# Performance work log

Hardware: AMD Instinct MI355X
Metric: run time of the kernel (lower is better)

## Reference

```python
import jax, jax.numpy as jnp
import numpy as np

B, OP, MA, F_IN, F_OUT = 8, 400, 200, 64, 64


def setup_inputs() -> dict:
    key = jax.random.key(0)
    ks = jax.random.split(key, 8)
    x = jax.random.normal(ks[0], (B, OP, F_IN), dtype=jnp.float32)
    y = jax.random.normal(ks[1], (B, MA, F_IN), dtype=jnp.float32)
    z = jax.random.normal(ks[2], (B, OP, MA, F_IN), dtype=jnp.float32)
    op_ma_adj = jax.random.randint(ks[3], (B, OP, MA), 0, 2, dtype=jnp.int32)
    # xavier-uniform-ish params
    lim = float(np.sqrt(6.0 / (F_IN + F_OUT)))
    W_op = jax.random.uniform(ks[4], (F_IN, F_OUT), minval=-lim, maxval=lim, dtype=jnp.float32)
    W_ma = jax.random.uniform(ks[5], (F_IN, F_OUT), minval=-lim, maxval=lim, dtype=jnp.float32)
    W_edge = jax.random.uniform(ks[6], (F_IN, F_OUT), minval=-lim, maxval=lim, dtype=jnp.float32)
    lim_a = float(np.sqrt(6.0 / (1 + 3 * F_OUT)))
    att_vec = jax.random.uniform(ks[7], (3 * F_OUT,), minval=-lim_a, maxval=lim_a, dtype=jnp.float32)
    return {"x": x, "y": y, "z": z, "op_ma_adj": op_ma_adj,
            "W_op": W_op, "W_ma": W_ma, "W_edge": W_edge, "att_vec": att_vec}


def reference(x, y, z, op_ma_adj, W_op, W_ma, W_edge, att_vec):
    F = W_op.shape[1]
    h_op = jnp.einsum('bni,io->bno', x, W_op)                      # [B, op, F]
    h = jnp.einsum('bmi,io->bmo', y, W_ma)                         # [B, ma, F]
    h_edge = jnp.einsum('bnmi,io->bnmo', z, W_edge).transpose(0, 2, 1, 3)  # [B, ma, op, F]
    # attention score: concat([h_op, h_ma, h_edge]) @ a  ==  per-part dot products (no BxMAxOPx3F materialization)
    a_op, a_ma, a_edge = att_vec[:F], att_vec[F:2 * F], att_vec[2 * F:]
    e = (jnp.einsum('bnf,f->bn', h_op, a_op)[:, None, :]
         + jnp.einsum('bmf,f->bm', h, a_ma)[:, :, None]
         + jnp.einsum('bmnf,f->bmn', h_edge, a_edge))              # [B, ma, op]
    e = jax.nn.leaky_relu(e, negative_slope=0.01)
    adjT = op_ma_adj.transpose(0, 2, 1)                            # [B, ma, op]
    row_empty = jnp.all(adjT == 0, axis=-1, keepdims=True)         # [B, ma, 1]
    att = jnp.where(adjT > 0, e, -jnp.inf)
    att = jnp.where(row_empty, 0.0, att)                           # empty rows -> uniform softmax (matches torch)
    att = jax.nn.softmax(att, axis=-1)                             # [B, ma, op]
    h_op_edge = h_op[:, None, :, :] + h_edge                       # [B, ma, op, F]
    h_prime = jnp.einsum('bmn,bmnf->bmf', att, h_op_edge)          # [B, ma, F]
    h_prime = jnp.where(row_empty, 0.0, h_prime) + h
    return jax.nn.elu(h_prime)
```

## Files before the change

kernel.cpp:

```cpp
#include <hip/hip_runtime.h>
#include <math.h>

#define B_   8
#define OP_  400
#define MA_  200
#define ZROW (MA_ * 64)
#define NEGM -1.0e30f

typedef float v4f __attribute__((ext_vector_type(4)));

__global__ __launch_bounds__(256) void precompute_k(
    const float* __restrict__ x, const float* __restrict__ y,
    const float* __restrict__ Wop, const float* __restrict__ Wma,
    const float* __restrict__ Wedge, const float* __restrict__ att,
    float* __restrict__ ws_we, float* __restrict__ ws_eop, float* __restrict__ ws_ema)
{
    __shared__ float w_s[192];
    const int tid = threadIdx.x, wv = tid >> 6, ln = tid & 63;
    if (tid < 192) {
        const int which = tid >> 6, i = tid & 63;
        const float* W = (which == 0) ? Wop : ((which == 1) ? Wma : Wedge);
        const float* a = att + which * 64;
        float acc = 0.f;
        #pragma unroll 8
        for (int f = 0; f < 64; ++f) acc = fmaf(W[i * 64 + f], a[f], acc);
        w_s[tid] = acc;
    }
    __syncthreads();
    if (blockIdx.x == 0 && tid < 64) ws_we[tid] = w_s[128 + tid];

    const int row = blockIdx.x * 4 + wv;
    if (row < B_ * OP_) {
        float s = x[(size_t)row * 64 + ln] * w_s[ln];
        #pragma unroll
        for (int o = 32; o > 0; o >>= 1) s += __shfl_xor(s, o, 64);
        if (ln == 0) ws_eop[row] = s;
    } else if (row < B_ * OP_ + B_ * MA_) {
        const int r2 = row - B_ * OP_;
        float s = y[(size_t)r2 * 64 + ln] * w_s[64 + ln];
        #pragma unroll
        for (int o = 32; o > 0; o >>= 1) s += __shfl_xor(s, o, 64);
        if (ln == 0) ws_ema[r2] = s;
    }
}

__global__ __launch_bounds__(256) void gat_fused(
    const float* __restrict__ x, const float* __restrict__ y,
    const float* __restrict__ z, const int* __restrict__ adj,
    const float* __restrict__ Wop, const float* __restrict__ Wma,
    const float* __restrict__ Wedge,
    const float* __restrict__ ws_we, const float* __restrict__ ws_eop,
    const float* __restrict__ ws_ema, float* __restrict__ out)
{
    __shared__ int   ln_s[4][112];
    __shared__ float le_s[4][112];
    __shared__ float mred[4], lred[4];
    __shared__ float vws[4][64], uws[4][64];
    __shared__ float vs_s[64], us_s[64], ys_s[64];
    __shared__ float pvt[4][64];

    const int tid = threadIdx.x, wv = tid >> 6, ln = tid & 63;
    const int g = ln >> 4, q = ln & 15;
    const int bm = blockIdx.x;
    const int b = bm / MA_, m = bm % MA_;

    const float ema = ws_ema[bm];

    const int rbase = wv * 100;
    int cnt = 0;
    #pragma unroll
    for (int round = 0; round < 2; ++round) {
        const int lr = round * 64 + ln;
        const int n  = rbase + lr;
        bool a = false;
        if (lr < 100) a = (adj[((size_t)(b * OP_ + n)) * MA_ + m] != 0);
        const unsigned long long mask = __ballot(a);
        if (a) {
            const int pos = cnt + __popcll(mask & ((1ull << ln) - 1ull));
            ln_s[wv][pos] = n;
            le_s[wv][pos] = ws_eop[b * OP_ + n] + ema;
        }
        cnt += __popcll(mask);
    }
    const int cnt_p = (cnt + 7) & ~7;
    if (ln < cnt_p - cnt) {
        ln_s[wv][cnt + ln] = rbase;
        le_s[wv][cnt + ln] = NEGM;
    }

    const float* zP = z + ((size_t)b * OP_ * MA_ + m) * 64;
    const float* xP = x + (size_t)b * OP_ * 64;
    const v4f wq = ((const v4f*)ws_we)[q];

    v4f v = {0.f, 0.f, 0.f, 0.f}, u = {0.f, 0.f, 0.f, 0.f};
    float M = NEGM, L = 0.f;

    #define UPD(z4, x4, eo) do {                                               \
        float s_ = fmaf((z4).x, wq.x, fmaf((z4).y, wq.y,                       \
                   fmaf((z4).z, wq.z, (z4).w * wq.w)));                        \
        s_ += __shfl_xor(s_, 1, 64); s_ += __shfl_xor(s_, 2, 64);              \
        s_ += __shfl_xor(s_, 4, 64); s_ += __shfl_xor(s_, 8, 64);              \
        float e_ = s_ + (eo);                                                  \
        e_ = (e_ >= 0.f) ? e_ : 0.01f * e_;                                    \
        const float m2_ = fmaxf(M, e_);                                        \
        const float c_  = __expf(M - m2_);                                     \
        const float p_  = __expf(e_ - m2_);                                    \
        L = fmaf(L, c_, p_);                                                   \
        v = v * c_ + (z4) * p_;                                                \
        u = u * c_ + (x4) * p_;                                                \
        M = m2_;                                                               \
    } while (0)

    for (int i = 0; i < cnt_p; i += 8) {
        const int na = ln_s[wv][i + g];
        const int nb = ln_s[wv][i + 4 + g];
        const float ea = le_s[wv][i + g];
        const float eb = le_s[wv][i + 4 + g];
        const v4f za = __builtin_nontemporal_load(
            (const v4f*)(zP + (size_t)na * ZROW) + q);
        const v4f zb4 = __builtin_nontemporal_load(
            (const v4f*)(zP + (size_t)nb * ZROW) + q);
        const v4f xa  = *((const v4f*)(xP + ((size_t)na << 6)) + q);
        const v4f xb4 = *((const v4f*)(xP + ((size_t)nb << 6)) + q);
        UPD(za, xa, ea);
        UPD(zb4, xb4, eb);
    }
    #undef UPD

    float Mw = M;
    Mw = fmaxf(Mw, __shfl_xor(Mw, 16, 64));
    Mw = fmaxf(Mw, __shfl_xor(Mw, 32, 64));
    const float cg = __expf(M - Mw);
    float Lw = L * cg;
    Lw += __shfl_xor(Lw, 16, 64);
    Lw += __shfl_xor(Lw, 32, 64);
    v *= cg;
    u *= cg;
    v.x += __shfl_xor(v.x, 16, 64); v.y += __shfl_xor(v.y, 16, 64);
    v.z += __shfl_xor(v.z, 16, 64); v.w += __shfl_xor(v.w, 16, 64);
    v.x += __shfl_xor(v.x, 32, 64); v.y += __shfl_xor(v.y, 32, 64);
    v.z += __shfl_xor(v.z, 32, 64); v.w += __shfl_xor(v.w, 32, 64);
    u.x += __shfl_xor(u.x, 16, 64); u.y += __shfl_xor(u.y, 16, 64);
    u.z += __shfl_xor(u.z, 16, 64); u.w += __shfl_xor(u.w, 16, 64);
    u.x += __shfl_xor(u.x, 32, 64); u.y += __shfl_xor(u.y, 32, 64);
    u.z += __shfl_xor(u.z, 32, 64); u.w += __shfl_xor(u.w, 32, 64);

    if (ln < 16) {
        ((v4f*)vws[wv])[q] = v;
        ((v4f*)uws[wv])[q] = u;
    }
    if (ln == 0) { mred[wv] = Mw; lred[wv] = Lw; }
    __syncthreads();

    if (tid < 64) {
        const float Mg = fmaxf(fmaxf(mred[0], mred[1]), fmaxf(mred[2], mred[3]));
        const float c0 = __expf(mred[0] - Mg);
        const float c1 = __expf(mred[1] - Mg);
        const float c2 = __expf(mred[2] - Mg);
        const float c3 = __expf(mred[3] - Mg);
        const float Lg = c0 * lred[0] + c1 * lred[1] + c2 * lred[2] + c3 * lred[3];
        const float inv = (Lg > 0.f) ? (1.f / Lg) : 0.f;
        vs_s[tid] = (c0 * vws[0][tid] + c1 * vws[1][tid] +
                     c2 * vws[2][tid] + c3 * vws[3][tid]) * inv;
        us_s[tid] = (c0 * uws[0][tid] + c1 * uws[1][tid] +
                     c2 * uws[2][tid] + c3 * uws[3][tid]) * inv;
        ys_s[tid] = y[(size_t)bm * 64 + tid];
    }
    __syncthreads();

    {
        float acc = 0.f;
        const int i0 = wv * 16;
        #pragma unroll
        for (int k = 0; k < 16; ++k) {
            const int i = i0 + k;
            acc += vs_s[i] * Wedge[i * 64 + ln]
                 + us_s[i] * Wop[i * 64 + ln]
                 + ys_s[i] * Wma[i * 64 + ln];
        }
        pvt[wv][ln] = acc;
    }
    __syncthreads();
    if (tid < 64) {
        const float h = pvt[0][tid] + pvt[1][tid] + pvt[2][tid] + pvt[3][tid];
        out[(size_t)bm * 64 + tid] = (h > 0.f) ? h : (__expf(h) - 1.f);
    }
}

extern "C" void kernel_launch(void* const* d_in, const int* in_sizes, int n_in,
                              void* d_out, int out_size, void* d_ws, size_t ws_size,
                              hipStream_t stream) {
    const float* x     = (const float*)d_in[0];
    const float* y     = (const float*)d_in[1];
    const float* z     = (const float*)d_in[2];
    const int*   adj   = (const int*)d_in[3];
    const float* Wop   = (const float*)d_in[4];
    const float* Wma   = (const float*)d_in[5];
    const float* Wedge = (const float*)d_in[6];
    const float* att   = (const float*)d_in[7];

    float* ws     = (float*)d_ws;
    float* ws_we  = ws;
    float* ws_eop = ws + 64;
    float* ws_ema = ws + 64 + B_ * OP_;

    precompute_k<<<1200, 256, 0, stream>>>(
        x, y, Wop, Wma, Wedge, att, ws_we, ws_eop, ws_ema);
    gat_fused<<<B_ * MA_, 256, 0, stream>>>(
        x, y, z, adj, Wop, Wma, Wedge, ws_we, ws_eop, ws_ema, (float*)d_out);
}
```

Baseline: 240.1 us.

## Prefetch next gather rows and split online softmax into dual accumulators

The main loop now loads the z and x rows for the next iteration into registers before processing the current ones, so global memory latency overlaps with compute. Each wave keeps two independent online-softmax states (max, sum, v, u), which shortens the serial dependency chain; they are merged once after the loop. The per-step rescale uses a single exp chosen by comparison instead of two exps. Neighbour index and logit are packed into one int2 LDS entry, and the padding is extended by 8 entries so the prefetch can read safely past the end. The cost is extra register pressure from the duplicated accumulators and the prefetch buffers.

```diff
diff --git a/kernel.cpp b/kernel.cpp
--- a/kernel.cpp
+++ b/kernel.cpp
@@ -52,8 +52,7 @@
     const float* __restrict__ ws_we, const float* __restrict__ ws_eop,
     const float* __restrict__ ws_ema, float* __restrict__ out)
 {
-    __shared__ int   ln_s[4][112];
-    __shared__ float le_s[4][112];
+    __shared__ int2  nle[4][112];
     __shared__ float mred[4], lred[4];
     __shared__ float vws[4][64], uws[4][64];
     __shared__ float vs_s[64], us_s[64], ys_s[64];
@@ -77,55 +76,67 @@
         const unsigned long long mask = __ballot(a);
         if (a) {
             const int pos = cnt + __popcll(mask & ((1ull << ln) - 1ull));
-            ln_s[wv][pos] = n;
-            le_s[wv][pos] = ws_eop[b * OP_ + n] + ema;
+            nle[wv][pos] = make_int2(n, __float_as_int(ws_eop[b * OP_ + n] + ema));
         }
         cnt += __popcll(mask);
     }
     const int cnt_p = (cnt + 7) & ~7;
-    if (ln < cnt_p - cnt) {
-        ln_s[wv][cnt + ln] = rbase;
-        le_s[wv][cnt + ln] = NEGM;
+    if (ln < cnt_p + 8 - cnt) {
+        nle[wv][cnt + ln] = make_int2(rbase, __float_as_int(NEGM));
     }
 
     const float* zP = z + ((size_t)b * OP_ * MA_ + m) * 64;
     const float* xP = x + (size_t)b * OP_ * 64;
     const v4f wq = ((const v4f*)ws_we)[q];
 
-    v4f v = {0.f, 0.f, 0.f, 0.f}, u = {0.f, 0.f, 0.f, 0.f};
-    float M = NEGM, L = 0.f;
-
-    #define UPD(z4, x4, eo) do {                                               \
-        float s_ = fmaf((z4).x, wq.x, fmaf((z4).y, wq.y,                       \
-                   fmaf((z4).z, wq.z, (z4).w * wq.w)));                        \
-        s_ += __shfl_xor(s_, 1, 64); s_ += __shfl_xor(s_, 2, 64);              \
-        s_ += __shfl_xor(s_, 4, 64); s_ += __shfl_xor(s_, 8, 64);              \
-        float e_ = s_ + (eo);                                                  \
-        e_ = (e_ >= 0.f) ? e_ : 0.01f * e_;                                    \
-        const float m2_ = fmaxf(M, e_);                                        \
-        const float c_  = __expf(M - m2_);                                     \
-        const float p_  = __expf(e_ - m2_);                                    \
-        L = fmaf(L, c_, p_);                                                   \
-        v = v * c_ + (z4) * p_;                                                \
-        u = u * c_ + (x4) * p_;                                                \
-        M = m2_;                                                               \
-    } while (0)
+    v4f v0 = {0.f,0.f,0.f,0.f}, u0 = {0.f,0.f,0.f,0.f};
+    v4f v1 = {0.f,0.f,0.f,0.f}, u1 = {0.f,0.f,0.f,0.f};
+    float M0 = NEGM, L0 = 0.f, M1 = NEGM, L1 = 0.f;
+
+    auto upd = [&wq](float& M, float& L, v4f& v, v4f& u,
+                     const v4f z4, const v4f x4, const float eo) {
+        float s_ = fmaf(z4.x, wq.x, fmaf(z4.y, wq.y,
+                   fmaf(z4.z, wq.z, z4.w * wq.w)));
+        s_ += __shfl_xor(s_, 1, 64); s_ += __shfl_xor(s_, 2, 64);
+        s_ += __shfl_xor(s_, 4, 64); s_ += __shfl_xor(s_, 8, 64);
+        float e_ = s_ + eo;
+        e_ = (e_ >= 0.f) ? e_ : 0.01f * e_;
+        const float m2_ = fmaxf(M, e_);
+        const float w_  = __expf(fminf(M, e_) - m2_);
+        const bool  nm  = (e_ > M);
+        const float c_  = nm ? w_ : 1.f;
+        const float p_  = nm ? 1.f : w_;
+        L = fmaf(L, c_, p_);
+        v = v * c_ + z4 * p_;
+        u = u * c_ + x4 * p_;
+        M = m2_;
+    };
+
+    int2 pa = nle[wv][g];
+    int2 pb = nle[wv][4 + g];
+    v4f za = __builtin_nontemporal_load((const v4f*)(zP + (size_t)pa.x * ZROW) + q);
+    v4f zb = __builtin_nontemporal_load((const v4f*)(zP + (size_t)pb.x * ZROW) + q);
+    v4f xa = *((const v4f*)(xP + ((size_t)pa.x << 6)) + q);
+    v4f xb = *((const v4f*)(xP + ((size_t)pb.x << 6)) + q);
 
     for (int i = 0; i < cnt_p; i += 8) {
-        const int na = ln_s[wv][i + g];
-        const int nb = ln_s[wv][i + 4 + g];
-        const float ea = le_s[wv][i + g];
-        const float eb = le_s[wv][i + 4 + g];
-        const v4f za = __builtin_nontemporal_load(
-            (const v4f*)(zP + (size_t)na * ZROW) + q);
-        const v4f zb4 = __builtin_nontemporal_load(
-            (const v4f*)(zP + (size_t)nb * ZROW) + q);
-        const v4f xa  = *((const v4f*)(xP + ((size_t)na << 6)) + q);
-        const v4f xb4 = *((const v4f*)(xP + ((size_t)nb << 6)) + q);
-        UPD(za, xa, ea);
-        UPD(zb4, xb4, eb);
-    }
-    #undef UPD
+        const int2 qa = nle[wv][i + 8 + g];
+        const int2 qb = nle[wv][i + 12 + g];
+        const v4f nza = __builtin_nontemporal_load((const v4f*)(zP + (size_t)qa.x * ZROW) + q);
+        const v4f nzb = __builtin_nontemporal_load((const v4f*)(zP + (size_t)qb.x * ZROW) + q);
+        const v4f nxa = *((const v4f*)(xP + ((size_t)qa.x << 6)) + q);
+        const v4f nxb = *((const v4f*)(xP + ((size_t)qb.x << 6)) + q);
+        upd(M0, L0, v0, u0, za, xa, __int_as_float(pa.y));
+        upd(M1, L1, v1, u1, zb, xb, __int_as_float(pb.y));
+        pa = qa; pb = qb; za = nza; zb = nzb; xa = nxa; xb = nxb;
+    }
+
+    const float Mp = fmaxf(M0, M1);
+    const float ca = __expf(M0 - Mp), cb = __expf(M1 - Mp);
+    float L = L0 * ca + L1 * cb;
+    v4f  v = v0 * ca + v1 * cb;
+    v4f  u = u0 * ca + u1 * cb;
+    float M = Mp;
 
     float Mw = M;
     Mw = fmaxf(Mw, __shfl_xor(Mw, 16, 64));
```

After: 237.0 us, median of 2. No clear change (-1.3%).
